# Performance work log

Measured on AMD Instinct MI355X. Metric: run time of the kernel, lower is better.

## Reference

```python
import jax, jax.numpy as jnp
from jax import lax
import numpy as np

T, B, D, H = 512, 256, 128, 256
SHIFT = 0.0


def setup_inputs() -> dict:
    key = jax.random.key(0)
    ks = jax.random.split(key, 11)
    s_in = 1.0 / np.sqrt(D + H)
    s_cl = 1.0 / np.sqrt(H)
    return {
        "inputs": jax.random.normal(ks[0], (T, B, D), dtype=jnp.float32),
        "Wf": jax.random.normal(ks[1], (H, D + H), dtype=jnp.float32) * s_in,
        "bf": jax.random.normal(ks[2], (H,), dtype=jnp.float32) * s_in,
        "Wi": jax.random.normal(ks[3], (H, D + H), dtype=jnp.float32) * s_in,
        "bi": jax.random.normal(ks[4], (H,), dtype=jnp.float32) * s_in,
        "Wg": jax.random.normal(ks[5], (H, D + H), dtype=jnp.float32) * s_in,
        "bg": jax.random.normal(ks[6], (H,), dtype=jnp.float32) * s_in,
        "Wo": jax.random.normal(ks[7], (H, D + H), dtype=jnp.float32) * s_in,
        "bo": jax.random.normal(ks[8], (H,), dtype=jnp.float32) * s_in,
        "Wc": jax.random.normal(ks[9], (1, H), dtype=jnp.float32) * s_cl,
        "bc": jax.random.normal(ks[10], (1,), dtype=jnp.float32) * s_cl,
    }


def reference(inputs, Wf, bf, Wi, bi, Wg, bg, Wo, bo, Wc, bc):
    # Fuse the four gate linears into one GEMM per step: [4H, D+H]
    W = jnp.concatenate([Wf, Wi, Wg, Wo], axis=0)
    b = jnp.concatenate([bf, bi, bg, bo], axis=0)
    h = W.shape[0] // 4
    batch = inputs.shape[1]

    def step(carry, x):
        hx, cx = carry
        combined = jnp.concatenate([x, hx], axis=1)      # [B, D+H]
        z = combined @ W.T + b                            # [B, 4H]
        f = jax.nn.sigmoid(z[:, 0 * h:1 * h])
        i = jax.nn.sigmoid(z[:, 1 * h:2 * h])
        g = jnp.tanh(z[:, 2 * h:3 * h])
        o = jax.nn.sigmoid(z[:, 3 * h:4 * h])
        cx = f * cx + i * g
        hx = o * jnp.tanh(cx)
        return (hx, cx), hx

    h0 = jnp.zeros((batch, h), dtype=inputs.dtype)
    c0 = jnp.zeros((batch, h), dtype=inputs.dtype)
    (hx, cx), hs = lax.scan(step, (h0, c0), inputs)       # hs: [T, B, H]

    logits = hs @ Wc.T + bc                               # [T, B, 1]
    probs = jax.nn.sigmoid(logits + SHIFT)
    return (jnp.concatenate([probs, 1.0 - probs], axis=-1), hx, cx)
```

## Files before the change

kernel.cpp:

```cpp
#include <hip/hip_runtime.h>
#include <hip/hip_bf16.h>


#define T_STEPS 512
#define BATCH   256
#define DIN     128
#define HID     256
#define KDIM    384
#define LDK     392
#define GRIDN   256
#define NPOLL   96

typedef __attribute__((ext_vector_type(8))) short short8;
typedef __attribute__((ext_vector_type(4))) short short4v;
typedef __attribute__((ext_vector_type(4))) float f32x4;

__device__ __forceinline__ unsigned short f2bf(float f) {
    unsigned u = __float_as_uint(f);
    unsigned r = (u + 0x7FFFu + ((u >> 16) & 1u)) >> 16;
    return (unsigned short)r;
}
__device__ __forceinline__ float bf2f(unsigned short s) {
    return __uint_as_float(((unsigned)s) << 16);
}
__device__ __forceinline__ float sigmoid_f(float x) {
    return 1.f / (1.f + __expf(-x));
}
__device__ __forceinline__ float tanh_f(float x) {
    float e = __expf(2.f * x);
    return 1.f - 2.f / (e + 1.f);
}
__device__ __forceinline__ void poll_load_sc0(const unsigned int* p, uint4& a,
                                              uint4& b, uint4& c, uint4& d) {
    asm volatile(
        "global_load_dwordx4 %0, %4, off sc0\n\t"
        "global_load_dwordx4 %1, %4, off offset:16 sc0\n\t"
        "global_load_dwordx4 %2, %4, off offset:32 sc0\n\t"
        "global_load_dwordx4 %3, %4, off offset:48 sc0\n\t"
        "s_waitcnt vmcnt(0)"
        : "=&v"(a), "=&v"(b), "=&v"(c), "=&v"(d) : "v"(p) : "memory");
}
__device__ __forceinline__ void poll_load_sc1(const unsigned int* p, uint4& a,
                                              uint4& b, uint4& c, uint4& d) {
    asm volatile(
        "global_load_dwordx4 %0, %4, off sc1\n\t"
        "global_load_dwordx4 %1, %4, off offset:16 sc1\n\t"
        "global_load_dwordx4 %2, %4, off offset:32 sc1\n\t"
        "global_load_dwordx4 %3, %4, off offset:48 sc1\n\t"
        "s_waitcnt vmcnt(0)"
        : "=&v"(a), "=&v"(b), "=&v"(c), "=&v"(d) : "v"(p) : "memory");
}
__device__ __forceinline__ void store_plain_u32(unsigned int* p, unsigned int v) {
    asm volatile("global_store_dword %0, %1, off" :: "v"(p), "v"(v) : "memory");
}
__device__ __forceinline__ void store_sc1_u32(unsigned int* p, unsigned int v) {
    asm volatile("global_store_dword %0, %1, off sc1" :: "v"(p), "v"(v) : "memory");
}
__device__ __forceinline__ unsigned pack2bf(unsigned lo, unsigned hi) {
    return (hi & 0xFFFF0000u) | (lo >> 16);
}
__device__ __forceinline__ bool tags_ok(const uint4& a, const uint4& b,
                                        const uint4& c, const uint4& d,
                                        unsigned tag) {
    return ((a.x ^ tag) & 0xFFFFu) == 0 && ((a.y ^ tag) & 0xFFFFu) == 0 &&
           ((a.z ^ tag) & 0xFFFFu) == 0 && ((a.w ^ tag) & 0xFFFFu) == 0 &&
           ((b.x ^ tag) & 0xFFFFu) == 0 && ((b.y ^ tag) & 0xFFFFu) == 0 &&
           ((b.z ^ tag) & 0xFFFFu) == 0 && ((b.w ^ tag) & 0xFFFFu) == 0 &&
           ((c.x ^ tag) & 0xFFFFu) == 0 && ((c.y ^ tag) & 0xFFFFu) == 0 &&
           ((c.z ^ tag) & 0xFFFFu) == 0 && ((c.w ^ tag) & 0xFFFFu) == 0 &&
           ((d.x ^ tag) & 0xFFFFu) == 0 && ((d.y ^ tag) & 0xFFFFu) == 0 &&
           ((d.z ^ tag) & 0xFFFFu) == 0 && ((d.w ^ tag) & 0xFFFFu) == 0;
}

__global__ __launch_bounds__(256) void pack_w(
    const float* __restrict__ Wf, const float* __restrict__ Wi,
    const float* __restrict__ Wg, const float* __restrict__ Wo,
    unsigned short* __restrict__ Wp) {
    int idx = blockIdx.x * 256 + threadIdx.x;
    int n = idx / KDIM;
    int k = idx - n * KDIM;
    int g = n >> 8, j = n & 255;
    const float* s = (g == 0) ? Wf : (g == 1) ? Wi : (g == 2) ? Wg : Wo;
    Wp[idx] = f2bf(s[j * KDIM + k]);
}

__global__ __launch_bounds__(256) void pack_b(
    const float* __restrict__ bf, const float* __restrict__ bi,
    const float* __restrict__ bg, const float* __restrict__ bo,
    float* __restrict__ bp) {
    int n = blockIdx.x * 256 + threadIdx.x;
    int g = n >> 8, j = n & 255;
    const float* s = (g == 0) ? bf : (g == 1) ? bi : (g == 2) ? bg : bo;
    bp[n] = s[j];
}

__global__ __launch_bounds__(256) void init_k(unsigned int* __restrict__ hxp) {
    int tid = blockIdx.x * 256 + threadIdx.x;
    hxp[tid] = 0u;
    hxp[65536 + tid] = 0u;
    hxp[131072 + tid] = 0u;
    hxp[196608 + tid] = 0u;
}

__global__ __launch_bounds__(256, 1) void lstm_persist(
    const float* __restrict__ X,
    const unsigned short* __restrict__ W,
    const float* __restrict__ bias,
    unsigned int* __restrict__ hxp,
    unsigned short* __restrict__ hist,
    float* __restrict__ out) {
    __shared__ __align__(16) unsigned short comb_s[16 * LDK];
    __shared__ __align__(16) float z_s[4 * 272];
    __shared__ __align__(16) char pad_s[50176];
    __shared__ int fastok_s;

    const int tid = threadIdx.x;
    const int bg = blockIdx.x & 15, jg = blockIdx.x >> 4;
    const int b0 = bg * 16, j0 = jg * 16;
    const int wave = tid >> 6, lane = tid & 63;
    const int l16 = lane & 15, quad = lane >> 4;
    const int bi = tid >> 4, jj = tid & 15;
    const int b = b0 + bi, j = j0 + jj;

    const unsigned short* wrow =
        W + (size_t)(wave * 256 + j0 + l16) * KDIM + quad * 8;
    short8 wb[12];
#pragma unroll
    for (int kt = 0; kt < 12; ++kt) wb[kt] = *(const short8*)(wrow + kt * 32);

    const float bs0 = bias[0 * HID + j];
    const float bs1 = bias[1 * HID + j];
    const float bs2 = bias[2 * HID + j];
    const float bs3 = bias[3 * HID + j];
    if (tid == 0) {
        fastok_s = 1;
        ((volatile char*)pad_s)[0] = 0;
    }

    float c_reg = 0.f;
    float h_final = 0.f;

    const unsigned short* arow = &comb_s[l16 * LDK + quad * 8];
    const int hrow = tid >> 4, hc = tid & 15;
    const int xr0 = tid >> 5, xc4 = tid & 31, xr1 = (tid + 256) >> 5;

    const float* xb = X + b0 * DIN;
    float4 xv0 = *(const float4*)(xb + xr0 * DIN + xc4 * 4);
    float4 xv1 = *(const float4*)(xb + xr1 * DIN + xc4 * 4);

    __syncthreads();

    for (int k = 0; k < T_STEPS; ++k) {
        const unsigned tag = (unsigned)k;
        const unsigned int* fb =
            hxp + (k & 1) * 65536 + (b0 + hrow) * HID + hc * 16;
        const unsigned int* sb = fb + 131072;
        uint4 a, bq, cq, d;
        const int usefast = fastok_s;

        {
            short4v r;
            r.x = (short)f2bf(xv0.x); r.y = (short)f2bf(xv0.y);
            r.z = (short)f2bf(xv0.z); r.w = (short)f2bf(xv0.w);
            *(short4v*)(&comb_s[xr0 * LDK + xc4 * 4]) = r;
            r.x = (short)f2bf(xv1.x); r.y = (short)f2bf(xv1.y);
            r.z = (short)f2bf(xv1.z); r.w = (short)f2bf(xv1.w);
            *(short4v*)(&comb_s[xr1 * LDK + xc4 * 4]) = r;
        }

        if (usefast) {
            int tries = NPOLL;
            bool ok = false;
            for (;;) {
                poll_load_sc0(fb, a, bq, cq, d);
                if (tags_ok(a, bq, cq, d, tag)) { ok = true; break; }
                if (--tries == 0) break;
            }
            if (!ok) {
                fastok_s = 0;
                for (;;) {
                    poll_load_sc1(sb, a, bq, cq, d);
                    if (tags_ok(a, bq, cq, d, tag)) break;
                    __builtin_amdgcn_s_sleep(1);
                }
            }
        } else {
            for (;;) {
                poll_load_sc1(sb, a, bq, cq, d);
                if (tags_ok(a, bq, cq, d, tag)) break;
                __builtin_amdgcn_s_sleep(1);
            }
        }

        {
            uint4 p0, p1;
            p0.x = pack2bf(a.x, a.y);   p0.y = pack2bf(a.z, a.w);
            p0.z = pack2bf(bq.x, bq.y); p0.w = pack2bf(bq.z, bq.w);
            p1.x = pack2bf(cq.x, cq.y); p1.y = pack2bf(cq.z, cq.w);
            p1.z = pack2bf(d.x, d.y);   p1.w = pack2bf(d.z, d.w);
            *(uint4*)(&comb_s[hrow * LDK + DIN + hc * 16]) = p0;
            *(uint4*)(&comb_s[hrow * LDK + DIN + hc * 16 + 8]) = p1;
        }
        __syncthreads();

        f32x4 acc0 = {0.f, 0.f, 0.f, 0.f}, acc1 = {0.f, 0.f, 0.f, 0.f};
#pragma unroll
        for (int kt = 0; kt < 6; ++kt) {
            short8 a0 = *(const short8*)(arow + (2 * kt) * 32);
            short8 a1 = *(const short8*)(arow + (2 * kt + 1) * 32);
            acc0 = __builtin_amdgcn_mfma_f32_16x16x32_bf16(a0, wb[2 * kt], acc0, 0, 0, 0);
            acc1 = __builtin_amdgcn_mfma_f32_16x16x32_bf16(a1, wb[2 * kt + 1], acc1, 0, 0, 0);
        }
#pragma unroll
        for (int r = 0; r < 4; ++r)
            z_s[wave * 272 + (quad * 4 + r) * 17 + l16] = acc0[r] + acc1[r];
        __syncthreads();

        float zf = z_s[0 * 272 + bi * 17 + jj] + bs0;
        float zi = z_s[1 * 272 + bi * 17 + jj] + bs1;
        float zg = z_s[2 * 272 + bi * 17 + jj] + bs2;
        float zo = z_s[3 * 272 + bi * 17 + jj] + bs3;
        float fg = sigmoid_f(zf);
        float ig = sigmoid_f(zi);
        float gg = tanh_f(zg);
        float og = sigmoid_f(zo);
        c_reg = fg * c_reg + ig * gg;
        float hval = og * tanh_f(c_reg);
        unsigned short hb = f2bf(hval);
        unsigned int hword = ((unsigned)hb << 16) | (unsigned)(k + 1);
        unsigned int* fdst = hxp + ((k + 1) & 1) * 65536 + b * HID + j;
        store_plain_u32(fdst, hword);
        store_sc1_u32(fdst + 131072, hword);
        hist[(size_t)k * BATCH * HID + b * HID + j] = hb;
        if (k + 1 < T_STEPS) {
            const float* xn = X + (size_t)(k + 1) * BATCH * DIN + b0 * DIN;
            xv0 = *(const float4*)(xn + xr0 * DIN + xc4 * 4);
            xv1 = *(const float4*)(xn + xr1 * DIN + xc4 * 4);
        } else {
            h_final = hval;
        }
    }

    out[T_STEPS * BATCH * 2 + b * HID + j] = h_final;
    out[T_STEPS * BATCH * 2 + BATCH * HID + b * HID + j] = c_reg;
}

__global__ __launch_bounds__(256) void probs_k(
    const unsigned short* __restrict__ hist, const float* __restrict__ Wc,
    const float* __restrict__ bc, float* __restrict__ out) {
    const int wave = threadIdx.x >> 6, lane = threadIdx.x & 63;
    const size_t row = (size_t)blockIdx.x * 4 + wave;
    const unsigned short* h = hist + row * HID;
    short4v hv = *(const short4v*)(h + lane * 4);
    const float4 wv = *(const float4*)(Wc + lane * 4);
    float p = bf2f((unsigned short)hv.x) * wv.x + bf2f((unsigned short)hv.y) * wv.y +
              bf2f((unsigned short)hv.z) * wv.z + bf2f((unsigned short)hv.w) * wv.w;
#pragma unroll
    for (int off = 32; off >= 1; off >>= 1) p += __shfl_down(p, off);
    if (lane == 0) {
        float prob = 1.f / (1.f + __expf(-(p + bc[0])));
        out[row * 2]     = prob;
        out[row * 2 + 1] = 1.f - prob;
    }
}

extern "C" void kernel_launch(void* const* d_in, const int* in_sizes, int n_in,
                              void* d_out, int out_size, void* d_ws, size_t ws_size,
                              hipStream_t stream) {
    const float* X  = (const float*)d_in[0];
    const float* Wf = (const float*)d_in[1];
    const float* bfp= (const float*)d_in[2];
    const float* Wi = (const float*)d_in[3];
    const float* bip= (const float*)d_in[4];
    const float* Wg = (const float*)d_in[5];
    const float* bgp= (const float*)d_in[6];
    const float* Wo = (const float*)d_in[7];
    const float* bop= (const float*)d_in[8];
    const float* Wc = (const float*)d_in[9];
    const float* bc = (const float*)d_in[10];
    float* out = (float*)d_out;

    char* ws = (char*)d_ws;
    unsigned short* Wpack = (unsigned short*)(ws);
    float* bias = (float*)(ws + 786432);
    unsigned int* hxp = (unsigned int*)(ws + 790528);
    unsigned short* hist = (unsigned short*)(ws + 1839104);

    pack_w<<<1536, 256, 0, stream>>>(Wf, Wi, Wg, Wo, Wpack);
    pack_b<<<4, 256, 0, stream>>>(bfp, bip, bgp, bop, bias);
    init_k<<<256, 256, 0, stream>>>(hxp);

    void* kargs[6] = {(void*)&X, (void*)&Wpack, (void*)&bias,
                      (void*)&hxp, (void*)&hist, (void*)&out};
    (void)hipLaunchCooperativeKernel((const void*)lstm_persist, dim3(GRIDN),
                                     dim3(256), kargs, 0, stream);

    probs_k<<<32768, 256, 0, stream>>>(hist, Wc, bc, out);
}
```

Baseline: 1.109 ms.

## Precompute next step's input-projection MFMAs off the recurrent critical path

The x·W_x part of each step's gate GEMM is now computed at the end of the previous step, after h has been published. The next timestep's x is staged into a double-buffered LDS region (LDK widened, padding shrunk), and X is prefetched two steps ahead. Only the h-dependent MFMAs stay between the poll and the gate math, which shortens the serial dependency chain per step. The flag/h store is also switched from a plain store to an sc0 store, which changes the cache behaviour of the fast polling path.

```diff
diff --git a/kernel.cpp b/kernel.cpp
--- a/kernel.cpp
+++ b/kernel.cpp
@@ -7,7 +7,7 @@
 #define DIN     128
 #define HID     256
 #define KDIM    384
-#define LDK     392
+#define LDK     520
 #define GRIDN   256
 #define NPOLL   96
 
@@ -50,8 +50,8 @@
         "s_waitcnt vmcnt(0)"
         : "=&v"(a), "=&v"(b), "=&v"(c), "=&v"(d) : "v"(p) : "memory");
 }
-__device__ __forceinline__ void store_plain_u32(unsigned int* p, unsigned int v) {
-    asm volatile("global_store_dword %0, %1, off" :: "v"(p), "v"(v) : "memory");
+__device__ __forceinline__ void store_sc0_u32(unsigned int* p, unsigned int v) {
+    asm volatile("global_store_dword %0, %1, off sc0" :: "v"(p), "v"(v) : "memory");
 }
 __device__ __forceinline__ void store_sc1_u32(unsigned int* p, unsigned int v) {
     asm volatile("global_store_dword %0, %1, off sc1" :: "v"(p), "v"(v) : "memory");
@@ -111,7 +111,7 @@
     float* __restrict__ out) {
     __shared__ __align__(16) unsigned short comb_s[16 * LDK];
     __shared__ __align__(16) float z_s[4 * 272];
-    __shared__ __align__(16) char pad_s[50176];
+    __shared__ __align__(16) char pad_s[46080];
     __shared__ int fastok_s;
 
     const int tid = threadIdx.x;
@@ -144,11 +144,30 @@
     const int hrow = tid >> 4, hc = tid & 15;
     const int xr0 = tid >> 5, xc4 = tid & 31, xr1 = (tid + 256) >> 5;
 
-    const float* xb = X + b0 * DIN;
-    float4 xv0 = *(const float4*)(xb + xr0 * DIN + xc4 * 4);
-    float4 xv1 = *(const float4*)(xb + xr1 * DIN + xc4 * 4);
-
+    {
+        const float* x0b = X + b0 * DIN;
+        float4 t0 = *(const float4*)(x0b + xr0 * DIN + xc4 * 4);
+        float4 t1 = *(const float4*)(x0b + xr1 * DIN + xc4 * 4);
+        short4v r;
+        r.x = (short)f2bf(t0.x); r.y = (short)f2bf(t0.y);
+        r.z = (short)f2bf(t0.z); r.w = (short)f2bf(t0.w);
+        *(short4v*)(&comb_s[xr0 * LDK + xc4 * 4]) = r;
+        r.x = (short)f2bf(t1.x); r.y = (short)f2bf(t1.y);
+        r.z = (short)f2bf(t1.z); r.w = (short)f2bf(t1.w);
+        *(short4v*)(&comb_s[xr1 * LDK + xc4 * 4]) = r;
+    }
+    float4 xv0 = *(const float4*)(X + (size_t)BATCH * DIN + b0 * DIN + xr0 * DIN + xc4 * 4);
+    float4 xv1 = *(const float4*)(X + (size_t)BATCH * DIN + b0 * DIN + xr1 * DIN + xc4 * 4);
     __syncthreads();
+
+    f32x4 acc_x0 = {0.f, 0.f, 0.f, 0.f}, acc_x1 = {0.f, 0.f, 0.f, 0.f};
+#pragma unroll
+    for (int kp = 0; kp < 2; ++kp) {
+        short8 a0 = *(const short8*)(arow + (2 * kp) * 32);
+        short8 a1 = *(const short8*)(arow + (2 * kp + 1) * 32);
+        acc_x0 = __builtin_amdgcn_mfma_f32_16x16x32_bf16(a0, wb[2 * kp], acc_x0, 0, 0, 0);
+        acc_x1 = __builtin_amdgcn_mfma_f32_16x16x32_bf16(a1, wb[2 * kp + 1], acc_x1, 0, 0, 0);
+    }
 
     for (int k = 0; k < T_STEPS; ++k) {
         const unsigned tag = (unsigned)k;
@@ -157,16 +176,6 @@
         const unsigned int* sb = fb + 131072;
         uint4 a, bq, cq, d;
         const int usefast = fastok_s;
-
-        {
-            short4v r;
-            r.x = (short)f2bf(xv0.x); r.y = (short)f2bf(xv0.y);
-            r.z = (short)f2bf(xv0.z); r.w = (short)f2bf(xv0.w);
-            *(short4v*)(&comb_s[xr0 * LDK + xc4 * 4]) = r;
-            r.x = (short)f2bf(xv1.x); r.y = (short)f2bf(xv1.y);
-            r.z = (short)f2bf(xv1.z); r.w = (short)f2bf(xv1.w);
-            *(short4v*)(&comb_s[xr1 * LDK + xc4 * 4]) = r;
-        }
 
         if (usefast) {
             int tries = NPOLL;
@@ -201,11 +210,21 @@
             *(uint4*)(&comb_s[hrow * LDK + DIN + hc * 16]) = p0;
             *(uint4*)(&comb_s[hrow * LDK + DIN + hc * 16 + 8]) = p1;
         }
+        if (k + 1 < T_STEPS) {
+            const int xoff = ((k + 1) & 1) ? 384 : 0;
+            short4v r;
+            r.x = (short)f2bf(xv0.x); r.y = (short)f2bf(xv0.y);
+            r.z = (short)f2bf(xv0.z); r.w = (short)f2bf(xv0.w);
+            *(short4v*)(&comb_s[xr0 * LDK + xoff + xc4 * 4]) = r;
+            r.x = (short)f2bf(xv1.x); r.y = (short)f2bf(xv1.y);
+            r.z = (short)f2bf(xv1.z); r.w = (short)f2bf(xv1.w);
+            *(short4v*)(&comb_s[xr1 * LDK + xoff + xc4 * 4]) = r;
+        }
         __syncthreads();
 
-        f32x4 acc0 = {0.f, 0.f, 0.f, 0.f}, acc1 = {0.f, 0.f, 0.f, 0.f};
-#pragma unroll
-        for (int kt = 0; kt < 6; ++kt) {
+        f32x4 acc0 = acc_x0, acc1 = acc_x1;
+#pragma unroll
+        for (int kt = 2; kt < 6; ++kt) {
             short8 a0 = *(const short8*)(arow + (2 * kt) * 32);
             short8 a1 = *(const short8*)(arow + (2 * kt + 1) * 32);
             acc0 = __builtin_amdgcn_mfma_f32_16x16x32_bf16(a0, wb[2 * kt], acc0, 0, 0, 0);
@@ -229,13 +248,26 @@
         unsigned short hb = f2bf(hval);
         unsigned int hword = ((unsigned)hb << 16) | (unsigned)(k + 1);
         unsigned int* fdst = hxp + ((k + 1) & 1) * 65536 + b * HID + j;
-        store_plain_u32(fdst, hword);
+        store_sc0_u32(fdst, hword);
         store_sc1_u32(fdst + 131072, hword);
         hist[(size_t)k * BATCH * HID + b * HID + j] = hb;
+
         if (k + 1 < T_STEPS) {
-            const float* xn = X + (size_t)(k + 1) * BATCH * DIN + b0 * DIN;
-            xv0 = *(const float4*)(xn + xr0 * DIN + xc4 * 4);
-            xv1 = *(const float4*)(xn + xr1 * DIN + xc4 * 4);
+            if (k + 2 < T_STEPS) {
+                const float* xn = X + (size_t)(k + 2) * BATCH * DIN + b0 * DIN;
+                xv0 = *(const float4*)(xn + xr0 * DIN + xc4 * 4);
+                xv1 = *(const float4*)(xn + xr1 * DIN + xc4 * 4);
+            }
+            const int xoff = ((k + 1) & 1) ? 384 : 0;
+            f32x4 ax0 = {0.f, 0.f, 0.f, 0.f}, ax1 = {0.f, 0.f, 0.f, 0.f};
+#pragma unroll
+            for (int kp = 0; kp < 2; ++kp) {
+                short8 a0 = *(const short8*)(arow + xoff + (2 * kp) * 32);
+                short8 a1 = *(const short8*)(arow + xoff + (2 * kp + 1) * 32);
+                ax0 = __builtin_amdgcn_mfma_f32_16x16x32_bf16(a0, wb[2 * kp], ax0, 0, 0, 0);
+                ax1 = __builtin_amdgcn_mfma_f32_16x16x32_bf16(a1, wb[2 * kp + 1], ax1, 0, 0, 0);
+            }
+            acc_x0 = ax0; acc_x1 = ax1;
         } else {
             h_final = hval;
         }
```

After: 1.102 ms. No clear change (-0.6%).
